# Optimization experiments

Measured on AMD Instinct MI355X. Metric: run time of the kernel, lower is better.

The kernel has to match this reference:

```python
import jax, jax.numpy as jnp
import numpy as np

TEMPERATURE = 0.07


def setup_inputs() -> dict:
    key = jax.random.key(0)
    k1, k2 = jax.random.split(key)
    features = jax.random.normal(k1, (8192, 512), dtype=jnp.float32)
    targets = jax.random.randint(k2, (8192,), 0, 100, dtype=jnp.int64)
    return {"features": features, "targets": targets}


def reference(features, targets):
    n = features.shape[0]
    # L2 normalize along feature dim (F.normalize, dim=1)
    feats = features / jnp.linalg.norm(features, axis=1, keepdims=True)
    # [N, N] similarity matrix
    sim = jnp.matmul(feats, feats.T) / TEMPERATURE
    # positive-pair mask (same label, excluding self)
    mask = (targets[:, None] == targets[None, :]).astype(sim.dtype)
    mask = mask - jnp.eye(n, dtype=sim.dtype)
    # log_prob = sim - log(sum_j exp(sim_ij)) ; denominator includes the diagonal,
    # exactly as in the torch code. logsumexp is the stable single-pass form.
    log_prob = sim - jax.nn.logsumexp(sim, axis=1, keepdims=True)
    mean_log_prob_pos = jnp.sum(mask * log_prob, axis=1) / jnp.sum(mask, axis=1)
    loss = -jnp.mean(mean_log_prob_pos)
    return loss
```

## Files before the change

### kernel.cpp

```cpp
#include <hip/hip_runtime.h>

#define BM 128
#define BN 128
#define NSPLIT 8
#define TEMP 0.07f

typedef __attribute__((ext_vector_type(4))) float f32x4;
typedef __attribute__((ext_vector_type(4))) int   i32x4;
typedef __attribute__((ext_vector_type(8))) int   i32x8;

__global__ __launch_bounds__(256) void knorm(const float* __restrict__ X,
                                             unsigned char* __restrict__ Fq, int D) {
  int row = blockIdx.x * 4 + (threadIdx.x >> 6);
  int lane = threadIdx.x & 63;
  const float4* xr = (const float4*)(X + (size_t)row * D);
  float4 a = xr[lane * 2];
  float4 b = xr[lane * 2 + 1];
  float ss = a.x*a.x + a.y*a.y + a.z*a.z + a.w*a.w
           + b.x*b.x + b.y*b.y + b.z*b.z + b.w*b.w;
  #pragma unroll
  for (int off = 1; off < 64; off <<= 1) ss += __shfl_xor(ss, off, 64);
  float r = rsqrtf(ss);
  int lo = 0, hi = 0;
  lo = __builtin_amdgcn_cvt_pk_fp8_f32(a.x*r, a.y*r, lo, false);
  lo = __builtin_amdgcn_cvt_pk_fp8_f32(a.z*r, a.w*r, lo, true);
  hi = __builtin_amdgcn_cvt_pk_fp8_f32(b.x*r, b.y*r, hi, false);
  hi = __builtin_amdgcn_cvt_pk_fp8_f32(b.z*r, b.w*r, hi, true);
  int2 o = make_int2(lo, hi);
  *(int2*)(Fq + (size_t)row * D + lane * 8) = o;
}

__global__ __launch_bounds__(256, 1)
void kmain(const unsigned char* __restrict__ F, const int* __restrict__ tgt,
           float* __restrict__ psum, float* __restrict__ pmask, int N, int D) {
  __shared__ __align__(16) unsigned char Bs[BN * 512];

  const int tid  = threadIdx.x;
  const int lane = tid & 63;
  const int wave = tid >> 6;
  const int quad = lane >> 4;
  const int l15  = lane & 15;

  const int rowblk   = blockIdx.x / NSPLIT;
  const int split    = blockIdx.x % NSPLIT;
  const int rowbase  = rowblk * BM;
  const int colbase0 = split * (N / NSPLIT);

  i32x8 af[2][4];
  #pragma unroll
  for (int mi = 0; mi < 2; ++mi) {
    const unsigned char* rp = F + (size_t)(rowbase + wave*32 + mi*16 + l15) * 512 + quad*32;
    #pragma unroll
    for (int ks = 0; ks < 4; ++ks) {
      i32x4 lo = *(const i32x4*)(rp + ks*128);
      i32x4 hi = *(const i32x4*)(rp + ks*128 + 16);
      af[mi][ks] = __builtin_shufflevector(lo, hi, 0,1,2,3,4,5,6,7);
    }
  }

  int trow[2][4];
  #pragma unroll
  for (int mi = 0; mi < 2; ++mi)
    #pragma unroll
    for (int r = 0; r < 4; ++r)
      trow[mi][r] = tgt[rowbase + wave*32 + mi*16 + quad*4 + r];

  float se[2][4], ms[2][4];
  #pragma unroll
  for (int mi = 0; mi < 2; ++mi)
    #pragma unroll
    for (int r = 0; r < 4; ++r) { se[mi][r] = 0.f; ms[mi][r] = 0.f; }

  const float C1 = (1.0f / TEMP) * 1.4426950408889634f;
  const float C0 = -C1;

  const int sw0 = (quad * 2) ^ (l15 & 7);
  const unsigned char* bp0 = Bs + l15*512 + sw0*16;
  const unsigned char* bp1 = Bs + l15*512 + (sw0 ^ 1)*16;

  const int CT = (N / NSPLIT) / BN;
  for (int ct = 0; ct < CT; ++ct) {
    const int colbase = colbase0 + ct * BN;

    f32x4 acc[2][8];
    #pragma unroll
    for (int mi = 0; mi < 2; ++mi)
      #pragma unroll
      for (int ni = 0; ni < 8; ++ni)
        acc[mi][ni] = (f32x4){0.f, 0.f, 0.f, 0.f};

    __syncthreads();
    #pragma unroll
    for (int it = 0; it < 16; ++it) {
      const int L   = it * 256 + tid;
      const int row = L >> 5;
      const int ks  = (L & 31) ^ (row & 7);
      const unsigned char* g = F + (size_t)(colbase + row) * 512 + ks * 16;
      __builtin_amdgcn_global_load_lds(
          (const __attribute__((address_space(1))) void*)g,
          (__attribute__((address_space(3))) void*)(Bs + L * 16), 16, 0, 0);
    }
    __syncthreads();

    #pragma unroll
    for (int ks = 0; ks < 4; ++ks) {
      #pragma unroll
      for (int ni = 0; ni < 8; ++ni) {
        i32x4 b0 = *(const i32x4*)(bp0 + ni*8192 + ks*128);
        i32x4 b1 = *(const i32x4*)(bp1 + ni*8192 + ks*128);
        i32x8 b = __builtin_shufflevector(b0, b1, 0,1,2,3,4,5,6,7);
        acc[0][ni] = __builtin_amdgcn_mfma_scale_f32_16x16x128_f8f6f4(
            af[0][ks], b, acc[0][ni], 0, 0, 0, 0x7F7F7F7F, 0, 0x7F7F7F7F);
        acc[1][ni] = __builtin_amdgcn_mfma_scale_f32_16x16x128_f8f6f4(
            af[1][ks], b, acc[1][ni], 0, 0, 0, 0x7F7F7F7F, 0, 0x7F7F7F7F);
      }
    }

    int tc[8];
    #pragma unroll
    for (int ni = 0; ni < 8; ++ni) tc[ni] = tgt[colbase + ni*16 + l15];
    #pragma unroll
    for (int mi = 0; mi < 2; ++mi)
      #pragma unroll
      for (int ni = 0; ni < 8; ++ni)
        #pragma unroll
        for (int r = 0; r < 4; ++r) {
          float v = acc[mi][ni][r];
          se[mi][r] += __builtin_amdgcn_exp2f(fmaf(v, C1, C0));
          if (tc[ni] == trow[mi][r]) ms[mi][r] += v;
        }
  }

  #pragma unroll
  for (int mi = 0; mi < 2; ++mi)
    #pragma unroll
    for (int r = 0; r < 4; ++r) {
      float s = se[mi][r], m = ms[mi][r];
      #pragma unroll
      for (int off = 1; off < 16; off <<= 1) {
        s += __shfl_xor(s, off, 64);
        m += __shfl_xor(m, off, 64);
      }
      if (l15 == 0) {
        int row = rowbase + wave*32 + mi*16 + quad*4 + r;
        psum[(size_t)split * N + row]  = s;
        pmask[(size_t)split * N + row] = m;
      }
    }
}

__global__ __launch_bounds__(256) void kfinal(
    const float* __restrict__ psum, const float* __restrict__ pmask,
    const int* __restrict__ tgt, float* __restrict__ out, int N) {
  __shared__ int h[128];
  __shared__ float wsum[4];
  const int tid = threadIdx.x;
  if (tid < 128) h[tid] = 0;
  __syncthreads();
  for (int i = tid; i < N; i += 256) atomicAdd(&h[tgt[i] & 127], 1);
  __syncthreads();

  const int i = blockIdx.x * 256 + tid;
  float s = 0.f, m = 0.f;
  #pragma unroll
  for (int sp = 0; sp < NSPLIT; ++sp) {
    s += psum[(size_t)sp * N + i];
    m += pmask[(size_t)sp * N + i];
  }
  const float invT = 1.0f / TEMP;
  float cnt = (float)(h[tgt[i] & 127] - 1);
  float term = (m - 1.0f) * invT / cnt - (logf(s) + invT);
  #pragma unroll
  for (int off = 1; off < 64; off <<= 1) term += __shfl_xor(term, off, 64);
  if ((tid & 63) == 0) wsum[tid >> 6] = term;
  __syncthreads();
  if (tid == 0)
    atomicAdd(out, -(wsum[0] + wsum[1] + wsum[2] + wsum[3]) / (float)N);
}

extern "C" void kernel_launch(void* const* d_in, const int* in_sizes, int n_in,
                              void* d_out, int out_size, void* d_ws, size_t ws_size,
                              hipStream_t stream) {
  const float* X  = (const float*)d_in[0];
  const int* tgt  = (const int*)d_in[1];
  float* out      = (float*)d_out;
  const int N = in_sizes[1];
  const int D = in_sizes[0] / N;

  char* w = (char*)d_ws;
  unsigned char* Fq = (unsigned char*)w;
  size_t off = (size_t)N * D;
  float* psum  = (float*)(w + off); off += (size_t)NSPLIT * N * sizeof(float);
  float* pmask = (float*)(w + off);

  hipMemsetAsync(d_out, 0, sizeof(float), stream);
  knorm<<<N / 4, 256, 0, stream>>>(X, Fq, D);
  kmain<<<(N / BM) * NSPLIT, 256, 0, stream>>>(Fq, tgt, psum, pmask, N, D);
  kfinal<<<N / 256, 256, 0, stream>>>(psum, pmask, tgt, out, N);
}
```

Baseline: 129.1 us.

## Double-buffer column tiles in LDS and cache column targets in shared memory

Splits each 128-column tile into two 64-column halves held in a double-buffered LDS array. The async global-to-LDS load of the next half is issued before the MFMAs on the current one, with a partial vmcnt wait, so global load latency overlaps compute instead of sitting behind two full barriers per tile. Column labels are staged once into shared memory rather than reloaded from global each tile. In exchange there are twice as many iterations with barriers each, and the epilogue works on smaller tiles.

After: 114.9 us. 11.0% less time.

```diff
diff --git a/kernel.cpp b/kernel.cpp
--- a/kernel.cpp
+++ b/kernel.cpp
@@ -2,6 +2,7 @@
 
 #define BM 128
 #define BN 128
+#define HBN 64
 #define NSPLIT 8
 #define TEMP 0.07f
 
@@ -33,7 +34,8 @@
 __global__ __launch_bounds__(256, 1)
 void kmain(const unsigned char* __restrict__ F, const int* __restrict__ tgt,
            float* __restrict__ psum, float* __restrict__ pmask, int N, int D) {
-  __shared__ __align__(16) unsigned char Bs[BN * 512];
+  __shared__ __align__(16) unsigned char Bs[2][HBN * 512];
+  __shared__ int tgts[1024];
 
   const int tid  = threadIdx.x;
   const int lane = tid & 63;
@@ -45,6 +47,8 @@
   const int split    = blockIdx.x % NSPLIT;
   const int rowbase  = rowblk * BM;
   const int colbase0 = split * (N / NSPLIT);
+  const int NS       = N / NSPLIT;
+  const int GT       = NS / HBN;
 
   i32x8 af[2][4];
   #pragma unroll
@@ -65,6 +69,8 @@
     for (int r = 0; r < 4; ++r)
       trow[mi][r] = tgt[rowbase + wave*32 + mi*16 + quad*4 + r];
 
+  for (int i = tid; i < NS; i += 256) tgts[i] = tgt[colbase0 + i];
+
   float se[2][4], ms[2][4];
   #pragma unroll
   for (int mi = 0; mi < 2; ++mi)
@@ -74,38 +80,50 @@
   const float C1 = (1.0f / TEMP) * 1.4426950408889634f;
   const float C0 = -C1;
 
-  const int sw0 = (quad * 2) ^ (l15 & 7);
-  const unsigned char* bp0 = Bs + l15*512 + sw0*16;
-  const unsigned char* bp1 = Bs + l15*512 + (sw0 ^ 1)*16;
-
-  const int CT = (N / NSPLIT) / BN;
-  for (int ct = 0; ct < CT; ++ct) {
-    const int colbase = colbase0 + ct * BN;
-
-    f32x4 acc[2][8];
-    #pragma unroll
-    for (int mi = 0; mi < 2; ++mi)
-      #pragma unroll
-      for (int ni = 0; ni < 8; ++ni)
-        acc[mi][ni] = (f32x4){0.f, 0.f, 0.f, 0.f};
-
-    __syncthreads();
-    #pragma unroll
-    for (int it = 0; it < 16; ++it) {
+  auto STAGE = [&](int g, int buf) {
+    const int cb = colbase0 + g * HBN;
+    #pragma unroll
+    for (int it = 0; it < 8; ++it) {
       const int L   = it * 256 + tid;
       const int row = L >> 5;
       const int ks  = (L & 31) ^ (row & 7);
-      const unsigned char* g = F + (size_t)(colbase + row) * 512 + ks * 16;
+      const unsigned char* gp = F + (size_t)(cb + row) * 512 + ks * 16;
       __builtin_amdgcn_global_load_lds(
-          (const __attribute__((address_space(1))) void*)g,
-          (__attribute__((address_space(3))) void*)(Bs + L * 16), 16, 0, 0);
-    }
-    __syncthreads();
+          (const __attribute__((address_space(1))) void*)gp,
+          (__attribute__((address_space(3))) void*)(&Bs[buf][0] + L * 16), 16, 0, 0);
+    }
+  };
+
+  const int sw0 = (quad * 2) ^ (l15 & 7);
+
+  __syncthreads();
+
+  STAGE(0, 0);
+
+  for (int g = 0; g < GT; ++g) {
+    if (g + 1 < GT) {
+      STAGE(g + 1, (g + 1) & 1);
+      asm volatile("s_waitcnt vmcnt(8)" ::: "memory");
+    } else {
+      asm volatile("s_waitcnt vmcnt(0)" ::: "memory");
+    }
+    __builtin_amdgcn_s_barrier();
+
+    f32x4 acc[2][4];
+    #pragma unroll
+    for (int mi = 0; mi < 2; ++mi)
+      #pragma unroll
+      for (int ni = 0; ni < 4; ++ni)
+        acc[mi][ni] = (f32x4){0.f, 0.f, 0.f, 0.f};
+
+    const unsigned char* bb  = &Bs[0][0] + (g & 1) * (HBN * 512) + l15 * 512;
+    const unsigned char* bp0 = bb + sw0 * 16;
+    const unsigned char* bp1 = bb + (sw0 ^ 1) * 16;
 
     #pragma unroll
     for (int ks = 0; ks < 4; ++ks) {
       #pragma unroll
-      for (int ni = 0; ni < 8; ++ni) {
+      for (int ni = 0; ni < 4; ++ni) {
         i32x4 b0 = *(const i32x4*)(bp0 + ni*8192 + ks*128);
         i32x4 b1 = *(const i32x4*)(bp1 + ni*8192 + ks*128);
         i32x8 b = __builtin_shufflevector(b0, b1, 0,1,2,3,4,5,6,7);
@@ -115,14 +133,15 @@
             af[1][ks], b, acc[1][ni], 0, 0, 0, 0x7F7F7F7F, 0, 0x7F7F7F7F);
       }
     }
-
-    int tc[8];
-    #pragma unroll
-    for (int ni = 0; ni < 8; ++ni) tc[ni] = tgt[colbase + ni*16 + l15];
+    __builtin_amdgcn_s_barrier();
+
+    int tc[4];
+    #pragma unroll
+    for (int ni = 0; ni < 4; ++ni) tc[ni] = tgts[g*HBN + ni*16 + l15];
     #pragma unroll
     for (int mi = 0; mi < 2; ++mi)
       #pragma unroll
-      for (int ni = 0; ni < 8; ++ni)
+      for (int ni = 0; ni < 4; ++ni)
         #pragma unroll
         for (int r = 0; r < 4; ++r) {
           float v = acc[mi][ni][r];
```
